# Optimization experiments

Measured on AMD Instinct MI355X. Metric: run time of the kernel, lower is better.

Reference implementation:

```python
import jax, jax.numpy as jnp
import numpy as np

N_NODES = 100000
N_EDGES = 3200000
D = 128


def setup_inputs() -> dict:
    key = jax.random.key(0)
    ks = jax.random.split(key, 8)
    x = jax.random.normal(ks[0], (N_NODES, D), dtype=jnp.float32)
    edge_row = jax.random.randint(ks[1], (N_EDGES,), 0, N_NODES, dtype=jnp.int32)
    edge_col = jax.random.randint(ks[2], (N_EDGES,), 0, N_NODES, dtype=jnp.int32)
    edge_val = jax.random.uniform(ks[3], (N_EDGES,), dtype=jnp.float32)
    s = 1.0 / np.sqrt(D)  # nn.Linear default init scale
    W = jax.random.uniform(ks[4], (D, D), dtype=jnp.float32, minval=-s, maxval=s)
    b = jax.random.uniform(ks[5], (D,), dtype=jnp.float32, minval=-s, maxval=s)
    W_self = jax.random.uniform(ks[6], (D, D), dtype=jnp.float32, minval=-s, maxval=s)
    b_self = jax.random.uniform(ks[7], (D,), dtype=jnp.float32, minval=-s, maxval=s)
    return {"x": x, "edge_row": edge_row, "edge_col": edge_col, "edge_val": edge_val,
            "W": W, "b": b, "W_self": W_self, "b_self": b_self}


def reference(x, edge_row, edge_col, edge_val, W, b, W_self, b_self):
    # x2 = ll_self(x); y = ll(x)   (torch Linear: x @ W.T + b)
    x2 = x @ W_self.T + b_self                      # [N, D]
    y = x @ W.T + b                                 # [N, D]
    # torch.spmm(adj, y): out[r] = sum_e val[e] * y[col[e]] for edges with row[e]==r
    msgs = edge_val[:, None] * y[edge_col]          # [E, D] gather
    agg = jax.ops.segment_sum(msgs, edge_row, num_segments=N_NODES)  # [N, D] scatter-add
    return jax.nn.relu(agg + x2)
```

## Files before the change

### kernel.cpp

```cpp
#include <hip/hip_runtime.h>
#include <hip/hip_bf16.h>

#define D 128
#define SCAN_CHUNK 1024

typedef __attribute__((ext_vector_type(8))) short short8v;
typedef __attribute__((ext_vector_type(4))) float floatx4;

__device__ inline short f2bf(float f) {
    union { float f; unsigned u; } v; v.f = f;
    unsigned r = v.u + 0x7fffu + ((v.u >> 16) & 1u);
    return (short)(r >> 16);
}
__device__ inline float bf2f(short h) {
    union { unsigned u; float f; } v;
    v.u = ((unsigned)(unsigned short)h) << 16;
    return v.f;
}

__global__ __launch_bounds__(256) void convert_w(
    const float* __restrict__ W, const float* __restrict__ Ws,
    short* __restrict__ Whb)
{
    const int i = blockIdx.x * 256 + threadIdx.x;
    if (i < D * D) {
        Whb[i] = f2bf(W[i]);
        Whb[D * D + i] = f2bf(Ws[i]);
    }
}

__global__ __launch_bounds__(256) void gemm_mfma(
    const float* __restrict__ x, const short* __restrict__ Whb,
    const float* __restrict__ bW, const float* __restrict__ bs,
    short* __restrict__ yh, float* __restrict__ out, int N)
{
    const int l  = threadIdx.x & 63;
    const int w  = threadIdx.x >> 6;
    const int r0 = blockIdx.x * 64 + w * 16;
    const int lr = l & 15;
    const int lk = l >> 4;

    const int arow = r0 + lr;
    const int arow_c = arow < N ? arow : N - 1;
    const float* xr = x + (size_t)arow_c * D;

    short8v afrag[4];
#pragma unroll
    for (int kc = 0; kc < 4; ++kc) {
        const float4 f0 = *(const float4*)(xr + kc * 32 + lk * 8);
        const float4 f1 = *(const float4*)(xr + kc * 32 + lk * 8 + 4);
        short8v a;
        a[0] = f2bf(f0.x); a[1] = f2bf(f0.y); a[2] = f2bf(f0.z); a[3] = f2bf(f0.w);
        a[4] = f2bf(f1.x); a[5] = f2bf(f1.y); a[6] = f2bf(f1.z); a[7] = f2bf(f1.w);
        afrag[kc] = a;
    }

#pragma unroll
    for (int ct = 0; ct < 16; ++ct) {
        const short* wrow = Whb + (size_t)(ct * 16 + lr) * D;
        floatx4 acc = {0.f, 0.f, 0.f, 0.f};
#pragma unroll
        for (int kc = 0; kc < 4; ++kc) {
            const short8v b = *(const short8v*)(wrow + kc * 32 + lk * 8);
            acc = __builtin_amdgcn_mfma_f32_16x16x32_bf16(afrag[kc], b, acc, 0, 0, 0);
        }
        const int col  = (ct & 7) * 16 + lr;
        const float bias = (ct < 8) ? bW[col] : bs[col];
#pragma unroll
        for (int r = 0; r < 4; ++r) {
            const int row = r0 + lk * 4 + r;
            if (row < N) {
                if (ct < 8) yh[(size_t)row * D + col] = f2bf(acc[r] + bias);
                else        out[(size_t)row * D + col] = acc[r] + bias;
            }
        }
    }
}

__global__ __launch_bounds__(256) void hist_kernel(
    const int* __restrict__ row, unsigned* __restrict__ cnt, int E)
{
    for (int e = blockIdx.x * blockDim.x + threadIdx.x; e < E;
         e += gridDim.x * blockDim.x)
        atomicAdd(&cnt[row[e]], 1u);
}

__global__ __launch_bounds__(256) void scan1_kernel(
    const unsigned* __restrict__ cnt, unsigned* __restrict__ chunkSum, int n)
{
    __shared__ unsigned s[256];
    const int b = blockIdx.x, t = threadIdx.x;
    const int base = b * SCAN_CHUNK + t * 4;
    unsigned tsum = 0;
#pragma unroll
    for (int i = 0; i < 4; ++i) {
        const int idx = base + i;
        if (idx < n) tsum += cnt[idx];
    }
    s[t] = tsum; __syncthreads();
    for (int off = 128; off > 0; off >>= 1) {
        if (t < off) s[t] += s[t + off];
        __syncthreads();
    }
    if (t == 0) chunkSum[b] = s[0];
}

__global__ __launch_bounds__(128) void scan2_kernel(
    const unsigned* __restrict__ chunkSum, unsigned* __restrict__ chunkBase, int nc)
{
    __shared__ unsigned s[128];
    const int t = threadIdx.x;
    const unsigned v = (t < nc) ? chunkSum[t] : 0u;
    s[t] = v; __syncthreads();
    for (int off = 1; off < 128; off <<= 1) {
        const unsigned u = (t >= off) ? s[t - off] : 0u;
        __syncthreads();
        s[t] += u;
        __syncthreads();
    }
    if (t < nc) chunkBase[t] = s[t] - v;
}

__global__ __launch_bounds__(256) void scan3_kernel(
    const unsigned* __restrict__ cnt, const unsigned* __restrict__ chunkBase,
    unsigned* __restrict__ rowStart, unsigned* __restrict__ cursor, int n)
{
    __shared__ unsigned s[256];
    const int b = blockIdx.x, t = threadIdx.x;
    const int base = b * SCAN_CHUNK + t * 4;
    unsigned v[4];
    unsigned tsum = 0;
#pragma unroll
    for (int i = 0; i < 4; ++i) {
        const int idx = base + i;
        v[i] = (idx < n) ? cnt[idx] : 0u;
        tsum += v[i];
    }
    s[t] = tsum; __syncthreads();
    for (int off = 1; off < 256; off <<= 1) {
        const unsigned u = (t >= off) ? s[t - off] : 0u;
        __syncthreads();
        s[t] += u;
        __syncthreads();
    }
    unsigned start = chunkBase[b] + (s[t] - tsum);
#pragma unroll
    for (int i = 0; i < 4; ++i) {
        const int idx = base + i;
        if (idx < n) { rowStart[idx] = start; cursor[idx] = start; }
        start += v[i];
    }
}

__global__ __launch_bounds__(256) void scatter_kernel(
    const int* __restrict__ row, const int* __restrict__ col,
    const float* __restrict__ val, unsigned* __restrict__ cursor,
    int2* __restrict__ pack, int E)
{
    for (int e = blockIdx.x * blockDim.x + threadIdx.x; e < E;
         e += gridDim.x * blockDim.x) {
        const int r = row[e];
        const unsigned p = atomicAdd(&cursor[r], 1u);
        pack[p] = make_int2(col[e], __float_as_int(val[e]));
    }
}

__global__ __launch_bounds__(256) void aggregate_kernel(
    const short* __restrict__ yh, const int2* __restrict__ pack,
    const unsigned* __restrict__ rowStart,
    float* __restrict__ out, int N, int E)
{
    const int wid = (int)((blockIdx.x * blockDim.x + threadIdx.x) >> 6);
    const int nw  = (int)((gridDim.x * blockDim.x) >> 6);
    const int l   = threadIdx.x & 63;
    const int g   = l >> 4;
    const int fl  = l & 15;

    for (int r = wid; r < N; r += nw) {
        const unsigned s0 = rowStart[r];
        const unsigned e1 = (r + 1 < N) ? rowStart[r + 1] : (unsigned)E;
        float acc[8] = {0.f, 0.f, 0.f, 0.f, 0.f, 0.f, 0.f, 0.f};

        unsigned e = s0;
        for (; e + 4 <= e1; e += 4) {
            const int2 p = pack[e + g];
            const float v = __int_as_float(p.y);
            const short8v yv = *(const short8v*)(yh + (size_t)p.x * D + fl * 8);
#pragma unroll
            for (int j = 0; j < 8; ++j) acc[j] += v * bf2f(yv[j]);
        }
        if (e < e1) {
            const unsigned idx = e + (unsigned)g;
            const bool act = idx < e1;
            int2 p = make_int2(0, 0);
            if (act) p = pack[idx];
            const float v = act ? __int_as_float(p.y) : 0.f;
            const short8v yv = *(const short8v*)(yh + (size_t)p.x * D + fl * 8);
#pragma unroll
            for (int j = 0; j < 8; ++j) acc[j] += v * bf2f(yv[j]);
        }

#pragma unroll
        for (int j = 0; j < 8; ++j) {
            acc[j] += __shfl_xor(acc[j], 16, 64);
            acc[j] += __shfl_xor(acc[j], 32, 64);
        }

        if (g == 0) {
            float* op = out + (size_t)r * D + fl * 8;
            const float4 x0 = *(const float4*)(op);
            const float4 x1 = *(const float4*)(op + 4);
            float4 o0, o1;
            o0.x = acc[0] + x0.x; o0.y = acc[1] + x0.y;
            o0.z = acc[2] + x0.z; o0.w = acc[3] + x0.w;
            o1.x = acc[4] + x1.x; o1.y = acc[5] + x1.y;
            o1.z = acc[6] + x1.z; o1.w = acc[7] + x1.w;
            o0.x = o0.x > 0.f ? o0.x : 0.f;  o0.y = o0.y > 0.f ? o0.y : 0.f;
            o0.z = o0.z > 0.f ? o0.z : 0.f;  o0.w = o0.w > 0.f ? o0.w : 0.f;
            o1.x = o1.x > 0.f ? o1.x : 0.f;  o1.y = o1.y > 0.f ? o1.y : 0.f;
            o1.z = o1.z > 0.f ? o1.z : 0.f;  o1.w = o1.w > 0.f ? o1.w : 0.f;
            *(float4*)(op)     = o0;
            *(float4*)(op + 4) = o1;
        }
    }
}

extern "C" void kernel_launch(void* const* d_in, const int* in_sizes, int n_in,
                              void* d_out, int out_size, void* d_ws, size_t ws_size,
                              hipStream_t stream)
{
    const float* x        = (const float*)d_in[0];
    const int*   edge_row = (const int*)  d_in[1];
    const int*   edge_col = (const int*)  d_in[2];
    const float* edge_val = (const float*)d_in[3];
    const float* W        = (const float*)d_in[4];
    const float* bW       = (const float*)d_in[5];
    const float* Ws       = (const float*)d_in[6];
    const float* bs       = (const float*)d_in[7];
    float* out = (float*)d_out;

    const int N = in_sizes[0] / D;
    const int E = in_sizes[1];
    const int NCHUNK = (N + SCAN_CHUNK - 1) / SCAN_CHUNK;

    short*    yh        = (short*)d_ws;
    short*    Whb       = yh + (size_t)N * D;
    unsigned* cnt       = (unsigned*)(Whb + 2 * D * D);
    unsigned* rowStart  = cnt + N;
    unsigned* cursor    = rowStart + N;
    unsigned* chunkSum  = cursor + N;
    unsigned* chunkBase = chunkSum + 128;
    int2*     pack      = (int2*)(chunkBase + 128);

    hipLaunchKernelGGL(convert_w, dim3((D * D + 255) / 256), dim3(256), 0, stream,
                       W, Ws, Whb);
    hipLaunchKernelGGL(gemm_mfma, dim3((N + 63) / 64), dim3(256), 0, stream,
                       x, Whb, bW, bs, yh, out, N);

    hipMemsetAsync(cnt, 0, (size_t)N * sizeof(unsigned), stream);
    hipLaunchKernelGGL(hist_kernel, dim3(2048), dim3(256), 0, stream,
                       edge_row, cnt, E);
    hipLaunchKernelGGL(scan1_kernel, dim3(NCHUNK), dim3(256), 0, stream,
                       cnt, chunkSum, N);
    hipLaunchKernelGGL(scan2_kernel, dim3(1), dim3(128), 0, stream,
                       chunkSum, chunkBase, NCHUNK);
    hipLaunchKernelGGL(scan3_kernel, dim3(NCHUNK), dim3(256), 0, stream,
                       cnt, chunkBase, rowStart, cursor, N);
    hipLaunchKernelGGL(scatter_kernel, dim3(2048), dim3(256), 0, stream,
                       edge_row, edge_col, edge_val, cursor, pack, E);

    hipLaunchKernelGGL(aggregate_kernel, dim3(4096), dim3(256), 0, stream,
                       yh, pack, rowStart, out, N, E);
}
```

Baseline: 691.2 us.

## Bucket edges by 64-row blocks and aggregate with shared-memory atomics

Replaces the per-row CSR build (global histogram, three-pass scan, per-edge global atomic scatter) with a coarse 64-row bucket sort. Histogramming and scatter use shared-memory counters with one global atomic per bucket per block, and the low row bits are packed into the column index. Aggregation gives one block per bucket and accumulates into a 64x128 fp32 shared tile with LDS float atomics before the fused residual-add and ReLU. This removes most global atomic traffic and the multi-kernel scan. In exchange it adds heavy LDS atomic contention, a 32KB LDS footprint that limits occupancy, narrower 4-byte gathers per lane, and hard limits on node count from MAXNB and the 17-bit column packing.

```diff
diff --git a/kernel.cpp b/kernel.cpp
--- a/kernel.cpp
+++ b/kernel.cpp
@@ -2,7 +2,9 @@
 #include <hip/hip_bf16.h>
 
 #define D 128
-#define SCAN_CHUNK 1024
+#define BROWS 64
+#define MAXNB 1600
+#define GRID_SC 250
 
 typedef __attribute__((ext_vector_type(8))) short short8v;
 typedef __attribute__((ext_vector_type(4))) float floatx4;
@@ -78,149 +80,130 @@
 }
 
 __global__ __launch_bounds__(256) void hist_kernel(
-    const int* __restrict__ row, unsigned* __restrict__ cnt, int E)
-{
-    for (int e = blockIdx.x * blockDim.x + threadIdx.x; e < E;
-         e += gridDim.x * blockDim.x)
-        atomicAdd(&cnt[row[e]], 1u);
-}
-
-__global__ __launch_bounds__(256) void scan1_kernel(
-    const unsigned* __restrict__ cnt, unsigned* __restrict__ chunkSum, int n)
+    const int* __restrict__ row, unsigned* __restrict__ cnt, int E, int nb)
+{
+    __shared__ unsigned h[MAXNB];
+    for (int i = threadIdx.x; i < nb; i += 256) h[i] = 0u;
+    __syncthreads();
+    for (int e = blockIdx.x * 256 + threadIdx.x; e < E; e += gridDim.x * 256)
+        atomicAdd(&h[(unsigned)row[e] >> 6], 1u);
+    __syncthreads();
+    for (int i = threadIdx.x; i < nb; i += 256) {
+        const unsigned v = h[i];
+        if (v) atomicAdd(&cnt[i], v);
+    }
+}
+
+__global__ __launch_bounds__(256) void scan_kernel(
+    const unsigned* __restrict__ cnt, unsigned* __restrict__ bucketStart,
+    unsigned* __restrict__ gCursor, int nb)
 {
     __shared__ unsigned s[256];
-    const int b = blockIdx.x, t = threadIdx.x;
-    const int base = b * SCAN_CHUNK + t * 4;
-    unsigned tsum = 0;
-#pragma unroll
-    for (int i = 0; i < 4; ++i) {
-        const int idx = base + i;
-        if (idx < n) tsum += cnt[idx];
-    }
-    s[t] = tsum; __syncthreads();
-    for (int off = 128; off > 0; off >>= 1) {
-        if (t < off) s[t] += s[t + off];
-        __syncthreads();
-    }
-    if (t == 0) chunkSum[b] = s[0];
-}
-
-__global__ __launch_bounds__(128) void scan2_kernel(
-    const unsigned* __restrict__ chunkSum, unsigned* __restrict__ chunkBase, int nc)
-{
-    __shared__ unsigned s[128];
     const int t = threadIdx.x;
-    const unsigned v = (t < nc) ? chunkSum[t] : 0u;
-    s[t] = v; __syncthreads();
-    for (int off = 1; off < 128; off <<= 1) {
-        const unsigned u = (t >= off) ? s[t - off] : 0u;
-        __syncthreads();
-        s[t] += u;
-        __syncthreads();
-    }
-    if (t < nc) chunkBase[t] = s[t] - v;
-}
-
-__global__ __launch_bounds__(256) void scan3_kernel(
-    const unsigned* __restrict__ cnt, const unsigned* __restrict__ chunkBase,
-    unsigned* __restrict__ rowStart, unsigned* __restrict__ cursor, int n)
-{
-    __shared__ unsigned s[256];
-    const int b = blockIdx.x, t = threadIdx.x;
-    const int base = b * SCAN_CHUNK + t * 4;
-    unsigned v[4];
-    unsigned tsum = 0;
-#pragma unroll
-    for (int i = 0; i < 4; ++i) {
-        const int idx = base + i;
-        v[i] = (idx < n) ? cnt[idx] : 0u;
-        tsum += v[i];
-    }
-    s[t] = tsum; __syncthreads();
+    unsigned loc[7];
+    unsigned sum = 0;
+#pragma unroll
+    for (int i = 0; i < 7; ++i) {
+        const int idx = t * 7 + i;
+        loc[i] = (idx < nb) ? cnt[idx] : 0u;
+        sum += loc[i];
+    }
+    s[t] = sum; __syncthreads();
     for (int off = 1; off < 256; off <<= 1) {
         const unsigned u = (t >= off) ? s[t - off] : 0u;
         __syncthreads();
         s[t] += u;
         __syncthreads();
     }
-    unsigned start = chunkBase[b] + (s[t] - tsum);
-#pragma unroll
-    for (int i = 0; i < 4; ++i) {
-        const int idx = base + i;
-        if (idx < n) { rowStart[idx] = start; cursor[idx] = start; }
-        start += v[i];
-    }
+    unsigned base = s[t] - sum;
+#pragma unroll
+    for (int i = 0; i < 7; ++i) {
+        const int idx = t * 7 + i;
+        if (idx < nb) { bucketStart[idx] = base; gCursor[idx] = base; }
+        base += loc[i];
+    }
+    if (t == 255) bucketStart[nb] = base;
 }
 
 __global__ __launch_bounds__(256) void scatter_kernel(
     const int* __restrict__ row, const int* __restrict__ col,
-    const float* __restrict__ val, unsigned* __restrict__ cursor,
-    int2* __restrict__ pack, int E)
-{
-    for (int e = blockIdx.x * blockDim.x + threadIdx.x; e < E;
-         e += gridDim.x * blockDim.x) {
-        const int r = row[e];
-        const unsigned p = atomicAdd(&cursor[r], 1u);
-        pack[p] = make_int2(col[e], __float_as_int(val[e]));
+    const float* __restrict__ val, unsigned* __restrict__ gCursor,
+    int2* __restrict__ pack, int E, int nb)
+{
+    __shared__ unsigned cntL[MAXNB];
+    __shared__ unsigned curL[MAXNB];
+    const int seg = (E + gridDim.x - 1) / gridDim.x;
+    const int s0  = blockIdx.x * seg;
+    const int s1  = min(E, s0 + seg);
+
+    for (int i = threadIdx.x; i < nb; i += 256) cntL[i] = 0u;
+    __syncthreads();
+    for (int e = s0 + threadIdx.x; e < s1; e += 256)
+        atomicAdd(&cntL[(unsigned)row[e] >> 6], 1u);
+    __syncthreads();
+    for (int i = threadIdx.x; i < nb; i += 256) {
+        const unsigned c = cntL[i];
+        curL[i] = c ? atomicAdd(&gCursor[i], c) : 0u;
+    }
+    __syncthreads();
+    for (int e = s0 + threadIdx.x; e < s1; e += 256) {
+        const unsigned r = (unsigned)row[e];
+        const unsigned pos = atomicAdd(&curL[r >> 6], 1u);
+        pack[pos] = make_int2(col[e] | (int)((r & 63u) << 17), __float_as_int(val[e]));
     }
 }
 
 __global__ __launch_bounds__(256) void aggregate_kernel(
     const short* __restrict__ yh, const int2* __restrict__ pack,
-    const unsigned* __restrict__ rowStart,
-    float* __restrict__ out, int N, int E)
-{
-    const int wid = (int)((blockIdx.x * blockDim.x + threadIdx.x) >> 6);
-    const int nw  = (int)((gridDim.x * blockDim.x) >> 6);
-    const int l   = threadIdx.x & 63;
-    const int g   = l >> 4;
-    const int fl  = l & 15;
-
-    for (int r = wid; r < N; r += nw) {
-        const unsigned s0 = rowStart[r];
-        const unsigned e1 = (r + 1 < N) ? rowStart[r + 1] : (unsigned)E;
-        float acc[8] = {0.f, 0.f, 0.f, 0.f, 0.f, 0.f, 0.f, 0.f};
-
-        unsigned e = s0;
-        for (; e + 4 <= e1; e += 4) {
-            const int2 p = pack[e + g];
-            const float v = __int_as_float(p.y);
-            const short8v yv = *(const short8v*)(yh + (size_t)p.x * D + fl * 8);
-#pragma unroll
-            for (int j = 0; j < 8; ++j) acc[j] += v * bf2f(yv[j]);
-        }
-        if (e < e1) {
-            const unsigned idx = e + (unsigned)g;
-            const bool act = idx < e1;
-            int2 p = make_int2(0, 0);
-            if (act) p = pack[idx];
-            const float v = act ? __int_as_float(p.y) : 0.f;
-            const short8v yv = *(const short8v*)(yh + (size_t)p.x * D + fl * 8);
-#pragma unroll
-            for (int j = 0; j < 8; ++j) acc[j] += v * bf2f(yv[j]);
-        }
-
-#pragma unroll
-        for (int j = 0; j < 8; ++j) {
-            acc[j] += __shfl_xor(acc[j], 16, 64);
-            acc[j] += __shfl_xor(acc[j], 32, 64);
-        }
-
-        if (g == 0) {
-            float* op = out + (size_t)r * D + fl * 8;
-            const float4 x0 = *(const float4*)(op);
-            const float4 x1 = *(const float4*)(op + 4);
-            float4 o0, o1;
-            o0.x = acc[0] + x0.x; o0.y = acc[1] + x0.y;
-            o0.z = acc[2] + x0.z; o0.w = acc[3] + x0.w;
-            o1.x = acc[4] + x1.x; o1.y = acc[5] + x1.y;
-            o1.z = acc[6] + x1.z; o1.w = acc[7] + x1.w;
-            o0.x = o0.x > 0.f ? o0.x : 0.f;  o0.y = o0.y > 0.f ? o0.y : 0.f;
-            o0.z = o0.z > 0.f ? o0.z : 0.f;  o0.w = o0.w > 0.f ? o0.w : 0.f;
-            o1.x = o1.x > 0.f ? o1.x : 0.f;  o1.y = o1.y > 0.f ? o1.y : 0.f;
-            o1.z = o1.z > 0.f ? o1.z : 0.f;  o1.w = o1.w > 0.f ? o1.w : 0.f;
-            *(float4*)(op)     = o0;
-            *(float4*)(op + 4) = o1;
+    const unsigned* __restrict__ bucketStart,
+    float* __restrict__ out, int N)
+{
+    __shared__ float acc[BROWS * D];
+    const int b = blockIdx.x;
+    const int t = threadIdx.x;
+    const int w = t >> 6;
+    const int l = t & 63;
+
+    {
+        float4* a4 = (float4*)acc;
+#pragma unroll
+        for (int i = 0; i < 8; ++i) a4[t + 256 * i] = make_float4(0.f, 0.f, 0.f, 0.f);
+    }
+    __syncthreads();
+
+    const unsigned eStart = bucketStart[b];
+    const unsigned eEnd   = bucketStart[b + 1];
+
+    for (unsigned e = eStart + (unsigned)w; e < eEnd; e += 4) {
+        const int2 p = pack[e];
+        const int  col = p.x & 0x1FFFF;
+        const int  rlo = (unsigned)p.x >> 17;
+        const float v  = __int_as_float(p.y);
+        const ushort2 yv = *(const ushort2*)(yh + (size_t)col * D + l * 2);
+        const float y0 = bf2f((short)yv.x);
+        const float y1 = bf2f((short)yv.y);
+        atomicAdd(&acc[rlo * D + l * 2],     v * y0);
+        atomicAdd(&acc[rlo * D + l * 2 + 1], v * y1);
+    }
+    __syncthreads();
+
+    const int rBase = b * BROWS;
+#pragma unroll
+    for (int i = 0; i < 8; ++i) {
+        const int idx4 = t + 256 * i;
+        const int rlo  = idx4 >> 5;
+        const int c4   = idx4 & 31;
+        const int r    = rBase + rlo;
+        if (r < N) {
+            float* op = out + (size_t)r * D + c4 * 4;
+            const float4 a = ((const float4*)acc)[idx4];
+            const float4 x2 = *(const float4*)op;
+            float4 o;
+            o.x = a.x + x2.x; o.y = a.y + x2.y;
+            o.z = a.z + x2.z; o.w = a.w + x2.w;
+            o.x = o.x > 0.f ? o.x : 0.f;  o.y = o.y > 0.f ? o.y : 0.f;
+            o.z = o.z > 0.f ? o.z : 0.f;  o.w = o.w > 0.f ? o.w : 0.f;
+            *(float4*)op = o;
         }
     }
 }
@@ -239,36 +222,30 @@
     const float* bs       = (const float*)d_in[7];
     float* out = (float*)d_out;
 
-    const int N = in_sizes[0] / D;
-    const int E = in_sizes[1];
-    const int NCHUNK = (N + SCAN_CHUNK - 1) / SCAN_CHUNK;
-
-    short*    yh        = (short*)d_ws;
-    short*    Whb       = yh + (size_t)N * D;
-    unsigned* cnt       = (unsigned*)(Whb + 2 * D * D);
-    unsigned* rowStart  = cnt + N;
-    unsigned* cursor    = rowStart + N;
-    unsigned* chunkSum  = cursor + N;
-    unsigned* chunkBase = chunkSum + 128;
-    int2*     pack      = (int2*)(chunkBase + 128);
+    const int N  = in_sizes[0] / D;
+    const int E  = in_sizes[1];
+    const int NB = (N + BROWS - 1) / BROWS;
+
+    short*    yh          = (short*)d_ws;
+    short*    Whb         = yh + (size_t)N * D;
+    unsigned* cnt         = (unsigned*)(Whb + 2 * D * D);
+    unsigned* bucketStart = cnt + MAXNB;
+    unsigned* gCursor     = bucketStart + MAXNB + 1;
+    int2*     pack        = (int2*)(gCursor + MAXNB);
 
     hipLaunchKernelGGL(convert_w, dim3((D * D + 255) / 256), dim3(256), 0, stream,
                        W, Ws, Whb);
     hipLaunchKernelGGL(gemm_mfma, dim3((N + 63) / 64), dim3(256), 0, stream,
                        x, Whb, bW, bs, yh, out, N);
 
-    hipMemsetAsync(cnt, 0, (size_t)N * sizeof(unsigned), stream);
-    hipLaunchKernelGGL(hist_kernel, dim3(2048), dim3(256), 0, stream,
-                       edge_row, cnt, E);
-    hipLaunchKernelGGL(scan1_kernel, dim3(NCHUNK), dim3(256), 0, stream,
-                       cnt, chunkSum, N);
-    hipLaunchKernelGGL(scan2_kernel, dim3(1), dim3(128), 0, stream,
-                       chunkSum, chunkBase, NCHUNK);
-    hipLaunchKernelGGL(scan3_kernel, dim3(NCHUNK), dim3(256), 0, stream,
-                       cnt, chunkBase, rowStart, cursor, N);
-    hipLaunchKernelGGL(scatter_kernel, dim3(2048), dim3(256), 0, stream,
-                       edge_row, edge_col, edge_val, cursor, pack, E);
-
-    hipLaunchKernelGGL(aggregate_kernel, dim3(4096), dim3(256), 0, stream,
-                       yh, pack, rowStart, out, N, E);
-}
+    hipMemsetAsync(cnt, 0, (size_t)NB * sizeof(unsigned), stream);
+    hipLaunchKernelGGL(hist_kernel, dim3(256), dim3(256), 0, stream,
+                       edge_row, cnt, E, NB);
+    hipLaunchKernelGGL(scan_kernel, dim3(1), dim3(256), 0, stream,
+                       cnt, bucketStart, gCursor, NB);
+    hipLaunchKernelGGL(scatter_kernel, dim3(GRID_SC), dim3(256), 0, stream,
+                       edge_row, edge_col, edge_val, gCursor, pack, E, NB);
+
+    hipLaunchKernelGGL(aggregate_kernel, dim3(NB), dim3(256), 0, stream,
+                       yh, pack, bucketStart, out, N);
+}
```

Result: slower. 2.653 ms (+283.9%).
